# Kernel optimization log

Measured on AMD Instinct MI355X. Metric: run time of the kernel, lower is better.

Reference implementation:

```python
import jax, jax.numpy as jnp
import numpy as np

N_NODES = 150000
N_EDGES = 300000
N_GRAPHS = 6000
HID = 256


def _lin_init(key, fan_in, fan_out):
    k1, k2 = jax.random.split(key)
    s = 1.0 / np.sqrt(fan_in)
    W = jax.random.uniform(k1, (fan_in, fan_out), jnp.float32, -s, s)
    b = jax.random.uniform(k2, (fan_out,), jnp.float32, -s, s)
    return W, b


def setup_inputs() -> dict:
    key = jax.random.key(0)
    ks = jax.random.split(key, 16)
    x = jax.random.normal(ks[0], (N_NODES, 7), jnp.float32)
    edge_index = jax.random.randint(ks[1], (2, N_EDGES), 0, N_NODES, jnp.int64)
    batch = jnp.sort(jax.random.randint(ks[2], (N_NODES,), 0, N_GRAPHS, jnp.int64))
    inp = {"x": x, "edge_index": edge_index, "batch": batch}
    dims_in = [7, HID, HID, HID]
    for i in range(4):
        Wa, ba = _lin_init(ks[3 + 2 * i], dims_in[i], HID)
        Wb, bb = _lin_init(ks[4 + 2 * i], HID, HID)
        inp[f"W{i+1}a"], inp[f"b{i+1}a"] = Wa, ba
        inp[f"W{i+1}b"], inp[f"b{i+1}b"] = Wb, bb
    inp["Wh1"], inp["bh1"] = _lin_init(ks[11], HID, 128)
    inp["Wh2"], inp["bh2"] = _lin_init(ks[12], 128, 3)
    return inp


def _gin_layer(x, src, dst, Wa, ba, Wb, bb):
    # sum-aggregate neighbor features: messages from src scattered to dst
    agg = jax.ops.segment_sum(x[src], dst, num_segments=N_NODES)
    h = agg + x  # (1 + eps) * x with eps = 0
    h = jax.nn.relu(h @ Wa + ba) @ Wb + bb  # GIN MLP
    return jax.nn.relu(h)  # outer F.relu in forward


def reference(x, edge_index, batch,
              W1a, b1a, W1b, b1b,
              W2a, b2a, W2b, b2b,
              W3a, b3a, W3b, b3b,
              W4a, b4a, W4b, b4b,
              Wh1, bh1, Wh2, bh2):
    src, dst = edge_index[0], edge_index[1]
    h = _gin_layer(x, src, dst, W1a, b1a, W1b, b1b)
    h = _gin_layer(h, src, dst, W2a, b2a, W2b, b2b)
    h = _gin_layer(h, src, dst, W3a, b3a, W3b, b3b)
    h = _gin_layer(h, src, dst, W4a, b4a, W4b, b4b)
    # global mean pool per graph
    sums = jax.ops.segment_sum(h, batch, num_segments=N_GRAPHS)
    counts = jax.ops.segment_sum(jnp.ones((N_NODES,), h.dtype), batch, num_segments=N_GRAPHS)
    pooled = sums / jnp.maximum(counts, 1.0)[:, None]
    # head (Dropout is identity in eval mode)
    out = jax.nn.relu(pooled @ Wh1 + bh1) @ Wh2 + bh2
    return out
```

## Files before the change

### kernel.cpp

```cpp
#include <hip/hip_runtime.h>

using bf16x8 = __attribute__((ext_vector_type(8))) __bf16;
using bf16x4 = __attribute__((ext_vector_type(4))) __bf16;
using f32x4  = __attribute__((ext_vector_type(4))) float;

#define MN    150000
#define NEDGE 300000
#define NG    6000
#define NSCAN 586

__device__ __forceinline__ float loadF(const void* p, size_t i, int f32) {
    return f32 ? ((const float*)p)[i] : (float)((const __bf16*)p)[i];
}
__device__ __forceinline__ int loadI(const int* p, size_t i, int i64) {
    return i64 ? p[2 * i] : p[i];
}

__global__ void k_probe(const void* W1a, const int* ei, const int* batch, int* flags) {
    __shared__ int s_f32, s_einz, s_bnz;
    if (threadIdx.x == 0) { s_f32 = 0; s_einz = 0; s_bnz = 0; }
    __syncthreads();
    const unsigned short* w = (const unsigned short*)W1a;
    for (int i = threadIdx.x; i < 1792; i += 256) {
        int e = (w[i] >> 7) & 0xFF;
        if (e >= 0xF0) s_f32 = 1;
    }
    for (int i = threadIdx.x; i < 2048; i += 256)
        if (ei[2 * i + 1] != 0) s_einz = 1;
    for (int i = threadIdx.x; i < 2048; i += 256)
        if (batch[75000 + 2 * i + 1] != 0) s_bnz = 1;
    __syncthreads();
    if (threadIdx.x == 0) {
        flags[0] = s_f32;
        flags[1] = s_einz ? 0 : 1;
        flags[2] = s_bnz ? 0 : 1;
    }
}

__global__ void k_zero_i32(int* p, int n) {
    int i = blockIdx.x * 256 + threadIdx.x;
    if (i < n) p[i] = 0;
}
__global__ void k_zero_f32(float* p, int n) {
    int i = blockIdx.x * 256 + threadIdx.x;
    if (i < n) p[i] = 0.f;
}

__global__ void k_cvtWT(const void* W0, const void* W1, const void* W2, const void* W3,
                        const void* W4, const void* W5, const void* W6,
                        __bf16* __restrict__ Wt, const int* __restrict__ flags) {
    int j = blockIdx.x >> 8;
    int n = blockIdx.x & 255, k = threadIdx.x;
    const void* Ws[7] = {W0, W1, W2, W3, W4, W5, W6};
    Wt[(size_t)j * 65536 + (size_t)n * 256 + k] = (__bf16)loadF(Ws[j], (size_t)k * 256 + n, flags[0]);
}

__global__ void k_deg(const int* __restrict__ ei, int* __restrict__ cnt, int nE,
                      const int* __restrict__ flags) {
    int e = blockIdx.x * 256 + threadIdx.x;
    if (e >= nE) return;
    int i64 = flags[1];
    int d = loadI(ei, (size_t)nE + e, i64);
    if ((unsigned)d >= (unsigned)MN) d = 0;
    atomicAdd(&cnt[d], 1);
}
__global__ void k_blksum(const int* __restrict__ cnt, int* __restrict__ bsum, int n) {
    __shared__ int s[256];
    int t = threadIdx.x;
    int i = blockIdx.x * 256 + t;
    s[t] = (i < n) ? cnt[i] : 0;
    __syncthreads();
    for (int o = 128; o > 0; o >>= 1) {
        if (t < o) s[t] += s[t + o];
        __syncthreads();
    }
    if (t == 0) bsum[blockIdx.x] = s[0];
}
__global__ __launch_bounds__(1024) void k_scanb(const int* __restrict__ bsum,
                                                int* __restrict__ bbase, int nb) {
    __shared__ int s[1024];
    int t = threadIdx.x;
    int v = (t < nb) ? bsum[t] : 0;
    s[t] = v;
    __syncthreads();
#pragma unroll
    for (int o = 1; o < 1024; o <<= 1) {
        int x = (t >= o) ? s[t - o] : 0;
        __syncthreads();
        s[t] += x;
        __syncthreads();
    }
    if (t < nb) bbase[t] = s[t] - v;
}
__global__ void k_blkscan(const int* __restrict__ cnt, const int* __restrict__ bbase,
                          int* __restrict__ offs, int n) {
    __shared__ int s[256];
    int t = threadIdx.x;
    int i = blockIdx.x * 256 + t;
    int v = (i < n) ? cnt[i] : 0;
    s[t] = v;
    __syncthreads();
    for (int o = 1; o < 256; o <<= 1) {
        int x = (t >= o) ? s[t - o] : 0;
        __syncthreads();
        s[t] += x;
        __syncthreads();
    }
    if (i < n) offs[i] = bbase[blockIdx.x] + s[t] - v;
}
__global__ void k_fill(const int* __restrict__ ei, const int* __restrict__ offs,
                       int* __restrict__ cur, int* __restrict__ elist, int nE,
                       const int* __restrict__ flags) {
    int e = blockIdx.x * 256 + threadIdx.x;
    if (e >= nE) return;
    int i64 = flags[1];
    int s = loadI(ei, (size_t)e, i64);
    int d = loadI(ei, (size_t)nE + e, i64);
    if ((unsigned)s >= (unsigned)MN) s = 0;
    if ((unsigned)d >= (unsigned)MN) d = 0;
    int pos = offs[d] + atomicAdd(&cur[d], 1);
    if ((unsigned)pos < (unsigned)NEDGE) elist[pos] = s;
}

__global__ __launch_bounds__(256) void k_l1lite(
    const void* __restrict__ x, const int* __restrict__ offs,
    const int* __restrict__ deg, const int* __restrict__ elist,
    float* __restrict__ agg7, const int* __restrict__ flags, int M_) {
    int f32 = flags[0];
    int t = threadIdx.x;
    int v = blockIdx.x * 32 + (t >> 3);
    int j = t & 7;
    if (v >= M_ || j >= 7) return;
    float s = loadF(x, (size_t)v * 7 + j, f32);
    int b = offs[v], d = min(deg[v], 1024);
    for (int e = 0; e < d; ++e) {
        int u = elist[b + e];
        if ((unsigned)u >= (unsigned)MN) u = 0;
        s += loadF(x, (size_t)u * 7 + j, f32);
    }
    agg7[(size_t)v * 8 + j] = s;
}

__device__ __forceinline__ void gemm_core128(const __bf16* lA, const __bf16* __restrict__ WT,
                                             int n0, int lm, int lq, f32x4 acc[4][8]) {
    const __bf16* wp = WT + (size_t)(n0 + lm) * 256 + lq * 8;
    bf16x8 wf[4], wn[4];
#pragma unroll
    for (int ci = 0; ci < 4; ++ci)
        wf[ci] = *(const bf16x8*)(wp + ci * 16 * 256);
#pragma unroll
    for (int kt = 0; kt < 8; ++kt) {
        if (kt < 7) {
#pragma unroll
            for (int ci = 0; ci < 4; ++ci)
                wn[ci] = *(const bf16x8*)(wp + ci * 16 * 256 + (kt + 1) * 32);
        }
        int sw = (((kt * 4 + lq) ^ (lm & 7)) << 3);
        bf16x8 xf[8];
#pragma unroll
        for (int mi = 0; mi < 8; ++mi)
            xf[mi] = *(const bf16x8*)(lA + (mi * 16 + lm) * 256 + sw);
#pragma unroll
        for (int ci = 0; ci < 4; ++ci)
#pragma unroll
            for (int mi = 0; mi < 8; ++mi)
                acc[ci][mi] = __builtin_amdgcn_mfma_f32_16x16x32_bf16(
                    wf[ci], xf[mi], acc[ci][mi], 0, 0, 0);
#pragma unroll
        for (int ci = 0; ci < 4; ++ci) wf[ci] = wn[ci];
    }
}

__device__ __forceinline__ void stage128_agg(const __bf16* __restrict__ H, __bf16* lA,
                                             const int* __restrict__ offs,
                                             const int* __restrict__ deg,
                                             const int* __restrict__ elist,
                                             int bm, int t, int M_) {
    int tc = t & 7;
    int rl = t >> 3;
#pragma unroll 1
    for (int p = 0; p < 4; ++p) {
        int r = p * 32 + rl;
        int gr = bm + r;
        if (gr >= M_) gr = M_ - 1;
        const __bf16* self = H + (size_t)gr * 256 + tc * 32;
        float acc[32];
        {
            bf16x8 v0 = *(const bf16x8*)(self + 0);
            bf16x8 v1 = *(const bf16x8*)(self + 8);
            bf16x8 v2 = *(const bf16x8*)(self + 16);
            bf16x8 v3 = *(const bf16x8*)(self + 24);
#pragma unroll
            for (int j = 0; j < 8; ++j) {
                acc[j]      = (float)v0[j];
                acc[8 + j]  = (float)v1[j];
                acc[16 + j] = (float)v2[j];
                acc[24 + j] = (float)v3[j];
            }
        }
        int b = offs[gr], d = min(deg[gr], 1024);
        for (int e = 0; e < d; ++e) {
            int u = elist[b + e];
            if ((unsigned)u >= (unsigned)MN) u = 0;
            const __bf16* nb = H + (size_t)u * 256 + tc * 32;
            bf16x8 n0 = *(const bf16x8*)(nb + 0);
            bf16x8 n1 = *(const bf16x8*)(nb + 8);
            bf16x8 n2 = *(const bf16x8*)(nb + 16);
            bf16x8 n3 = *(const bf16x8*)(nb + 24);
#pragma unroll
            for (int j = 0; j < 8; ++j) {
                acc[j]      += (float)n0[j];
                acc[8 + j]  += (float)n1[j];
                acc[16 + j] += (float)n2[j];
                acc[24 + j] += (float)n3[j];
            }
        }
#pragma unroll
        for (int q = 0; q < 4; ++q) {
            int c = tc * 4 + q;
            bf16x8 o;
#pragma unroll
            for (int j = 0; j < 8; ++j) o[j] = (__bf16)acc[q * 8 + j];
            *(bf16x8*)(lA + r * 256 + ((c ^ (r & 7)) << 3)) = o;
        }
    }
}

__device__ __forceinline__ void epi_to_lds(__bf16* lA, f32x4 acc[4][8], const void* bias,
                                           int n0, int lm, int lq, int f32) {
#pragma unroll
    for (int ci = 0; ci < 4; ++ci) {
        int n4 = n0 + ci * 16 + lq * 4;
        float b0 = loadF(bias, n4 + 0, f32), b1 = loadF(bias, n4 + 1, f32);
        float b2 = loadF(bias, n4 + 2, f32), b3 = loadF(bias, n4 + 3, f32);
#pragma unroll
        for (int mi = 0; mi < 8; ++mi) {
            int m = mi * 16 + lm;
            f32x4 a = acc[ci][mi];
            bf16x4 v;
            v[0] = (__bf16)fmaxf(a[0] + b0, 0.f);
            v[1] = (__bf16)fmaxf(a[1] + b1, 0.f);
            v[2] = (__bf16)fmaxf(a[2] + b2, 0.f);
            v[3] = (__bf16)fmaxf(a[3] + b3, 0.f);
            *(bf16x4*)(lA + m * 256 + (((n4 >> 3) ^ (m & 7)) << 3) + (n4 & 7)) = v;
        }
    }
}

__device__ __forceinline__ void lds_to_global(const __bf16* lA, __bf16* __restrict__ Y,
                                              int bm, int w, int lane, int M_) {
    int half = lane >> 5;
    int cc = lane & 31;
#pragma unroll
    for (int it = 0; it < 16; ++it) {
        int r = w * 32 + it * 2 + half;
        int gm = bm + r;
        if (gm < M_) {
            bf16x8 v = *(const bf16x8*)(lA + r * 256 + ((cc ^ (r & 7)) << 3));
            *(bf16x8*)(Y + (size_t)gm * 256 + cc * 8) = v;
        }
    }
}

__global__ __launch_bounds__(256, 2) void k_agg_mlp(
    const __bf16* __restrict__ H, const int* __restrict__ offs, const int* __restrict__ deg,
    const int* __restrict__ elist,
    const __bf16* __restrict__ WaT, const void* __restrict__ ba,
    const __bf16* __restrict__ WbT, const void* __restrict__ bb,
    __bf16* __restrict__ Y, int M_, const int* __restrict__ flags) {
    __shared__ __align__(16) __bf16 lA[128 * 256];
    int t = threadIdx.x;
    int f32 = flags[0];
    int bm = blockIdx.x * 128;
    int w = t >> 6, lane = t & 63, lm = lane & 15, lq = lane >> 4;
    int n0 = w * 64;

    stage128_agg(H, lA, offs, deg, elist, bm, t, M_);
    __syncthreads();

    {
        f32x4 acc[4][8] = {};
        gemm_core128(lA, WaT, n0, lm, lq, acc);
        __syncthreads();
        epi_to_lds(lA, acc, ba, n0, lm, lq, f32);
    }
    __syncthreads();

    f32x4 acc2[4][8] = {};
    gemm_core128(lA, WbT, n0, lm, lq, acc2);
    __syncthreads();
    epi_to_lds(lA, acc2, bb, n0, lm, lq, f32);
    __syncthreads();
    lds_to_global(lA, Y, bm, w, lane, M_);
}

__global__ __launch_bounds__(256, 2) void k_gemm1(
    const float* __restrict__ agg7, const void* __restrict__ W1a, const void* __restrict__ b1a,
    const __bf16* __restrict__ WT, const void* __restrict__ bias,
    __bf16* __restrict__ Y, int M_, const int* __restrict__ flags) {
    __shared__ __align__(16) __bf16 lA[128 * 256];
    __shared__ float sW[7 * 256];
    __shared__ float sB[256];
    int t = threadIdx.x;
    int f32 = flags[0];
    int bm = blockIdx.x * 128;
    int w = t >> 6, lane = t & 63, lm = lane & 15, lq = lane >> 4;
    int n0 = w * 64;

    sB[t] = loadF(b1a, t, f32);
#pragma unroll
    for (int k = 0; k < 7; ++k) sW[k * 256 + t] = loadF(W1a, (size_t)k * 256 + t, f32);
    __syncthreads();

    {
        int r = t >> 1;
        int gr = bm + r;
        if (gr >= M_) gr = M_ - 1;
        float a[7];
#pragma unroll
        for (int k = 0; k < 7; ++k) a[k] = agg7[(size_t)gr * 8 + k];
        int c0 = (t & 1) * 128;
#pragma unroll
        for (int s8 = 0; s8 < 16; ++s8) {
            bf16x8 o;
#pragma unroll
            for (int j = 0; j < 8; ++j) {
                int cc = c0 + s8 * 8 + j;
                float v = sB[cc];
#pragma unroll
                for (int k = 0; k < 7; ++k) v = fmaf(a[k], sW[k * 256 + cc], v);
                o[j] = (__bf16)fmaxf(v, 0.f);
            }
            int ch = (c0 >> 3) + s8;
            *(bf16x8*)(lA + r * 256 + ((ch ^ (r & 7)) << 3)) = o;
        }
    }
    __syncthreads();

    f32x4 acc[4][8] = {};
    gemm_core128(lA, WT, n0, lm, lq, acc);
    __syncthreads();
    epi_to_lds(lA, acc, bias, n0, lm, lq, f32);
    __syncthreads();
    lds_to_global(lA, Y, bm, w, lane, M_);
}

__global__ void k_pool(const __bf16* __restrict__ h, const int* __restrict__ batch,
                       float* __restrict__ pool, float* __restrict__ cnt, int M_,
                       const int* __restrict__ flags) {
    int f = threadIdx.x;
    int base = blockIdx.x * 32;
    if (base >= M_) return;
    int i64 = flags[2];
    int end = min(base + 32, M_);
    int g = loadI(batch, base, i64);
    if ((unsigned)g >= (unsigned)NG) g = 0;
    float acc = 0.f;
    int run = 0;
    for (int m = base; m < end; ++m) {
        int bm = loadI(batch, m, i64);
        if ((unsigned)bm >= (unsigned)NG) bm = 0;
        if (bm != g) {
            atomicAdd(&pool[(size_t)g * 256 + f], acc);
            if (f == 0) atomicAdd(&cnt[g], (float)run);
            g = bm; acc = 0.f; run = 0;
        }
        acc += (float)h[(size_t)m * 256 + f];
        run++;
    }
    atomicAdd(&pool[(size_t)g * 256 + f], acc);
    if (f == 0) atomicAdd(&cnt[g], (float)run);
}

__global__ void k_head(const float* __restrict__ pool, const float* __restrict__ cnt,
                       const void* __restrict__ Wh1, const void* __restrict__ bh1,
                       const void* __restrict__ Wh2, const void* __restrict__ bh2,
                       void* __restrict__ outv, const int* __restrict__ flags) {
    int g = blockIdx.x, n = threadIdx.x;
    int f32 = flags[0];
    __shared__ float p[256];
    __shared__ float hid[128];
    float inv = 1.0f / fmaxf(cnt[g], 1.0f);
    for (int k = n; k < 256; k += 128) p[k] = pool[(size_t)g * 256 + k] * inv;
    __syncthreads();
    float s = loadF(bh1, n, f32);
    for (int k = 0; k < 256; ++k) s = fmaf(p[k], loadF(Wh1, (size_t)k * 128 + n, f32), s);
    hid[n] = fmaxf(s, 0.f);
    __syncthreads();
    if (n < 3) {
        float o = loadF(bh2, n, f32);
        for (int k = 0; k < 128; ++k)
            o = fmaf(hid[k], loadF(Wh2, (size_t)k * 3 + n, f32), o);
        if (f32) ((float*)outv)[(size_t)g * 3 + n] = o;
        else     ((__bf16*)outv)[(size_t)g * 3 + n] = (__bf16)o;
    }
}

extern "C" void kernel_launch(void* const* d_in, const int* in_sizes, int n_in,
                              void* d_out, int out_size, void* d_ws, size_t ws_size,
                              hipStream_t stream) {
    const void* x     = d_in[0];
    const int*  ei    = (const int*)d_in[1];
    const int*  batch = (const int*)d_in[2];
    const void *W[4][2], *b[4][2];
    for (int l = 0; l < 4; ++l) {
        W[l][0] = d_in[3 + 4 * l];
        b[l][0] = d_in[4 + 4 * l];
        W[l][1] = d_in[5 + 4 * l];
        b[l][1] = d_in[6 + 4 * l];
    }
    const void* Wh1 = d_in[19];
    const void* bh1 = d_in[20];
    const void* Wh2 = d_in[21];
    const void* bh2 = d_in[22];

    char* p = (char*)d_ws;
    auto alloc = [&](size_t bytes) -> char* {
        char* r = p;
        p += (bytes + 255) & ~(size_t)255;
        return r;
    };
    __bf16* B1    = (__bf16*)alloc((size_t)MN * 256 * 2);
    __bf16* B2    = (__bf16*)alloc((size_t)MN * 256 * 2);
    __bf16* WT    = (__bf16*)alloc((size_t)7 * 256 * 256 * 2);
    float*  AGG7  = (float*)alloc((size_t)MN * 8 * 4);
    int*    offs  = (int*)alloc((size_t)MN * 4);
    int*    cnt   = (int*)alloc((size_t)MN * 4);
    int*    elist = (int*)alloc((size_t)NEDGE * 4);
    int*    bsum  = (int*)alloc((size_t)NSCAN * 4);
    int*    bbase = (int*)alloc((size_t)NSCAN * 4);
    float*  POOL  = (float*)alloc((size_t)NG * 256 * 4);
    float*  CNTF  = (float*)alloc((size_t)NG * 4);
    int*    flags = (int*)alloc(64);

    k_probe<<<1, 256, 0, stream>>>(W[0][0], ei, batch, flags);

    k_cvtWT<<<7 * 256, 256, 0, stream>>>(W[0][1], W[1][0], W[1][1], W[2][0], W[2][1],
                                         W[3][0], W[3][1], WT, flags);

    k_zero_i32<<<NSCAN, 256, 0, stream>>>(cnt, MN);
    k_deg<<<(NEDGE + 255) / 256, 256, 0, stream>>>(ei, cnt, NEDGE, flags);
    k_blksum<<<NSCAN, 256, 0, stream>>>(cnt, bsum, MN);
    k_scanb<<<1, 1024, 0, stream>>>(bsum, bbase, NSCAN);
    k_blkscan<<<NSCAN, 256, 0, stream>>>(cnt, bbase, offs, MN);
    k_zero_i32<<<NSCAN, 256, 0, stream>>>(cnt, MN);
    k_fill<<<(NEDGE + 255) / 256, 256, 0, stream>>>(ei, offs, cnt, elist, NEDGE, flags);

    k_zero_f32<<<(NG * 257 + 255) / 256, 256, 0, stream>>>(POOL, NG * 256 + NG);

    int gblocks = (MN + 127) / 128;

    k_l1lite<<<(MN + 31) / 32, 256, 0, stream>>>(x, offs, cnt, elist, AGG7, flags, MN);
    k_gemm1<<<gblocks, 256, 0, stream>>>(AGG7, W[0][0], b[0][0], WT , b[0][1],
                                         B1, MN, flags);

    __bf16* bin = B1;
    __bf16* bout = B2;
    for (int l = 1; l < 4; ++l) {
        const __bf16* WaT = WT + (size_t)(1 + 2 * (l - 1)) * 65536;
        const __bf16* WbT = WT + (size_t)(2 + 2 * (l - 1)) * 65536;
        k_agg_mlp<<<gblocks, 256, 0, stream>>>(bin, offs, cnt, elist,
                                               WaT, b[l][0], WbT, b[l][1], bout, MN, flags);
        __bf16* tmp = bin; bin = bout; bout = tmp;
    }

    k_pool<<<(MN + 31) / 32, 256, 0, stream>>>(bin, batch, POOL, CNTF, MN, flags);
    k_head<<<NG, 128, 0, stream>>>(POOL, CNTF, Wh1, bh1, Wh2, bh2, d_out, flags);
}
```

Baseline: 660.1 us.

## Halve row tile to 64 in fused agg-MLP kernels and unroll neighbor gather by two

Shrinks the row tile of the fused aggregation+MLP and first-layer GEMM kernels from 128 to 64 rows. This halves LDS use and accumulator registers so up to 4 blocks can be resident per CU instead of 2, and doubles the number of blocks. The neighbor-gather loop is also unrolled by two to keep more independent loads in flight. The cost is that each weight fragment is reused over fewer rows, so weight traffic from L2 per output row doubles.

```diff
diff --git a/kernel.cpp b/kernel.cpp
--- a/kernel.cpp
+++ b/kernel.cpp
@@ -141,8 +141,8 @@
     agg7[(size_t)v * 8 + j] = s;
 }
 
-__device__ __forceinline__ void gemm_core128(const __bf16* lA, const __bf16* __restrict__ WT,
-                                             int n0, int lm, int lq, f32x4 acc[4][8]) {
+__device__ __forceinline__ void gemm_core64(const __bf16* lA, const __bf16* __restrict__ WT,
+                                            int n0, int lm, int lq, f32x4 acc[4][4]) {
     const __bf16* wp = WT + (size_t)(n0 + lm) * 256 + lq * 8;
     bf16x8 wf[4], wn[4];
 #pragma unroll
@@ -156,14 +156,14 @@
                 wn[ci] = *(const bf16x8*)(wp + ci * 16 * 256 + (kt + 1) * 32);
         }
         int sw = (((kt * 4 + lq) ^ (lm & 7)) << 3);
-        bf16x8 xf[8];
-#pragma unroll
-        for (int mi = 0; mi < 8; ++mi)
+        bf16x8 xf[4];
+#pragma unroll
+        for (int mi = 0; mi < 4; ++mi)
             xf[mi] = *(const bf16x8*)(lA + (mi * 16 + lm) * 256 + sw);
 #pragma unroll
         for (int ci = 0; ci < 4; ++ci)
 #pragma unroll
-            for (int mi = 0; mi < 8; ++mi)
+            for (int mi = 0; mi < 4; ++mi)
                 acc[ci][mi] = __builtin_amdgcn_mfma_f32_16x16x32_bf16(
                     wf[ci], xf[mi], acc[ci][mi], 0, 0, 0);
 #pragma unroll
@@ -171,15 +171,15 @@
     }
 }
 
-__device__ __forceinline__ void stage128_agg(const __bf16* __restrict__ H, __bf16* lA,
-                                             const int* __restrict__ offs,
-                                             const int* __restrict__ deg,
-                                             const int* __restrict__ elist,
-                                             int bm, int t, int M_) {
+__device__ __forceinline__ void stage64_agg(const __bf16* __restrict__ H, __bf16* lA,
+                                            const int* __restrict__ offs,
+                                            const int* __restrict__ deg,
+                                            const int* __restrict__ elist,
+                                            int bm, int t, int M_) {
     int tc = t & 7;
     int rl = t >> 3;
 #pragma unroll 1
-    for (int p = 0; p < 4; ++p) {
+    for (int p = 0; p < 2; ++p) {
         int r = p * 32 + rl;
         int gr = bm + r;
         if (gr >= M_) gr = M_ - 1;
@@ -199,7 +199,31 @@
             }
         }
         int b = offs[gr], d = min(deg[gr], 1024);
-        for (int e = 0; e < d; ++e) {
+        int e = 0;
+        for (; e + 1 < d; e += 2) {
+            int u0 = elist[b + e];
+            int u1 = elist[b + e + 1];
+            if ((unsigned)u0 >= (unsigned)MN) u0 = 0;
+            if ((unsigned)u1 >= (unsigned)MN) u1 = 0;
+            const __bf16* nb0 = H + (size_t)u0 * 256 + tc * 32;
+            const __bf16* nb1 = H + (size_t)u1 * 256 + tc * 32;
+            bf16x8 a0 = *(const bf16x8*)(nb0 + 0);
+            bf16x8 a1 = *(const bf16x8*)(nb0 + 8);
+            bf16x8 a2 = *(const bf16x8*)(nb0 + 16);
+            bf16x8 a3 = *(const bf16x8*)(nb0 + 24);
+            bf16x8 c0 = *(const bf16x8*)(nb1 + 0);
+            bf16x8 c1 = *(const bf16x8*)(nb1 + 8);
+            bf16x8 c2 = *(const bf16x8*)(nb1 + 16);
+            bf16x8 c3 = *(const bf16x8*)(nb1 + 24);
+#pragma unroll
+            for (int j = 0; j < 8; ++j) {
+                acc[j]      += (float)a0[j] + (float)c0[j];
+                acc[8 + j]  += (float)a1[j] + (float)c1[j];
+                acc[16 + j] += (float)a2[j] + (float)c2[j];
+                acc[24 + j] += (float)a3[j] + (float)c3[j];
+            }
+        }
+        if (e < d) {
             int u = elist[b + e];
             if ((unsigned)u >= (unsigned)MN) u = 0;
             const __bf16* nb = H + (size_t)u * 256 + tc * 32;
@@ -226,15 +250,15 @@
     }
 }
 
-__device__ __forceinline__ void epi_to_lds(__bf16* lA, f32x4 acc[4][8], const void* bias,
-                                           int n0, int lm, int lq, int f32) {
+__device__ __forceinline__ void epi_to_lds64(__bf16* lA, f32x4 acc[4][4], const void* bias,
+                                             int n0, int lm, int lq, int f32) {
 #pragma unroll
     for (int ci = 0; ci < 4; ++ci) {
         int n4 = n0 + ci * 16 + lq * 4;
         float b0 = loadF(bias, n4 + 0, f32), b1 = loadF(bias, n4 + 1, f32);
         float b2 = loadF(bias, n4 + 2, f32), b3 = loadF(bias, n4 + 3, f32);
 #pragma unroll
-        for (int mi = 0; mi < 8; ++mi) {
+        for (int mi = 0; mi < 4; ++mi) {
             int m = mi * 16 + lm;
             f32x4 a = acc[ci][mi];
             bf16x4 v;
@@ -247,13 +271,13 @@
     }
 }
 
-__device__ __forceinline__ void lds_to_global(const __bf16* lA, __bf16* __restrict__ Y,
-                                              int bm, int w, int lane, int M_) {
+__device__ __forceinline__ void lds_to_global64(const __bf16* lA, __bf16* __restrict__ Y,
+                                                int bm, int w, int lane, int M_) {
     int half = lane >> 5;
     int cc = lane & 31;
 #pragma unroll
-    for (int it = 0; it < 16; ++it) {
-        int r = w * 32 + it * 2 + half;
+    for (int it = 0; it < 8; ++it) {
+        int r = w * 16 + it * 2 + half;
         int gm = bm + r;
         if (gm < M_) {
             bf16x8 v = *(const bf16x8*)(lA + r * 256 + ((cc ^ (r & 7)) << 3));
@@ -262,48 +286,48 @@
     }
 }
 
-__global__ __launch_bounds__(256, 2) void k_agg_mlp(
+__global__ __launch_bounds__(256, 4) void k_agg_mlp(
     const __bf16* __restrict__ H, const int* __restrict__ offs, const int* __restrict__ deg,
     const int* __restrict__ elist,
     const __bf16* __restrict__ WaT, const void* __restrict__ ba,
     const __bf16* __restrict__ WbT, const void* __restrict__ bb,
     __bf16* __restrict__ Y, int M_, const int* __restrict__ flags) {
-    __shared__ __align__(16) __bf16 lA[128 * 256];
+    __shared__ __align__(16) __bf16 lA[64 * 256];
     int t = threadIdx.x;
     int f32 = flags[0];
-    int bm = blockIdx.x * 128;
+    int bm = blockIdx.x * 64;
     int w = t >> 6, lane = t & 63, lm = lane & 15, lq = lane >> 4;
     int n0 = w * 64;
 
-    stage128_agg(H, lA, offs, deg, elist, bm, t, M_);
+    stage64_agg(H, lA, offs, deg, elist, bm, t, M_);
     __syncthreads();
 
     {
-        f32x4 acc[4][8] = {};
-        gemm_core128(lA, WaT, n0, lm, lq, acc);
-        __syncthreads();
-        epi_to_lds(lA, acc, ba, n0, lm, lq, f32);
-    }
-    __syncthreads();
-
-    f32x4 acc2[4][8] = {};
-    gemm_core128(lA, WbT, n0, lm, lq, acc2);
-    __syncthreads();
-    epi_to_lds(lA, acc2, bb, n0, lm, lq, f32);
-    __syncthreads();
-    lds_to_global(lA, Y, bm, w, lane, M_);
-}
-
-__global__ __launch_bounds__(256, 2) void k_gemm1(
+        f32x4 acc[4][4] = {};
+        gemm_core64(lA, WaT, n0, lm, lq, acc);
+        __syncthreads();
+        epi_to_lds64(lA, acc, ba, n0, lm, lq, f32);
+    }
+    __syncthreads();
+
+    f32x4 acc2[4][4] = {};
+    gemm_core64(lA, WbT, n0, lm, lq, acc2);
+    __syncthreads();
+    epi_to_lds64(lA, acc2, bb, n0, lm, lq, f32);
+    __syncthreads();
+    lds_to_global64(lA, Y, bm, w, lane, M_);
+}
+
+__global__ __launch_bounds__(256, 4) void k_gemm1(
     const float* __restrict__ agg7, const void* __restrict__ W1a, const void* __restrict__ b1a,
     const __bf16* __restrict__ WT, const void* __restrict__ bias,
     __bf16* __restrict__ Y, int M_, const int* __restrict__ flags) {
-    __shared__ __align__(16) __bf16 lA[128 * 256];
+    __shared__ __align__(16) __bf16 lA[64 * 256];
     __shared__ float sW[7 * 256];
     __shared__ float sB[256];
     int t = threadIdx.x;
     int f32 = flags[0];
-    int bm = blockIdx.x * 128;
+    int bm = blockIdx.x * 64;
     int w = t >> 6, lane = t & 63, lm = lane & 15, lq = lane >> 4;
     int n0 = w * 64;
 
@@ -313,15 +337,15 @@
     __syncthreads();
 
     {
-        int r = t >> 1;
+        int r = t >> 2;
         int gr = bm + r;
         if (gr >= M_) gr = M_ - 1;
         float a[7];
 #pragma unroll
         for (int k = 0; k < 7; ++k) a[k] = agg7[(size_t)gr * 8 + k];
-        int c0 = (t & 1) * 128;
-#pragma unroll
-        for (int s8 = 0; s8 < 16; ++s8) {
+        int c0 = (t & 3) * 64;
+#pragma unroll
+        for (int s8 = 0; s8 < 8; ++s8) {
             bf16x8 o;
 #pragma unroll
             for (int j = 0; j < 8; ++j) {
@@ -337,12 +361,12 @@
     }
     __syncthreads();
 
-    f32x4 acc[4][8] = {};
-    gemm_core128(lA, WT, n0, lm, lq, acc);
-    __syncthreads();
-    epi_to_lds(lA, acc, bias, n0, lm, lq, f32);
-    __syncthreads();
-    lds_to_global(lA, Y, bm, w, lane, M_);
+    f32x4 acc[4][4] = {};
+    gemm_core64(lA, WT, n0, lm, lq, acc);
+    __syncthreads();
+    epi_to_lds64(lA, acc, bias, n0, lm, lq, f32);
+    __syncthreads();
+    lds_to_global64(lA, Y, bm, w, lane, M_);
 }
 
 __global__ void k_pool(const __bf16* __restrict__ h, const int* __restrict__ batch,
@@ -448,7 +472,7 @@
 
     k_zero_f32<<<(NG * 257 + 255) / 256, 256, 0, stream>>>(POOL, NG * 256 + NG);
 
-    int gblocks = (MN + 127) / 128;
+    int gblocks = (MN + 63) / 64;
 
     k_l1lite<<<(MN + 31) / 32, 256, 0, stream>>>(x, offs, cnt, elist, AGG7, flags, MN);
     k_gemm1<<<gblocks, 256, 0, stream>>>(AGG7, W[0][0], b[0][0], WT , b[0][1],
```

Result: slower. 721.9 us (+9.4%).
